# Optimization experiments

Hardware: AMD Instinct MI355X
Metric: run time of the kernel (lower is better)

Reference implementation:

```python
import math
import jax, jax.numpy as jnp
import numpy as np

B, L, DIM, H = 2, 2048, 1024, 16
D = DIM // H  # head_dim = 64
EPS = 1e-6


def setup_inputs() -> dict:
    key = jax.random.key(0)
    ks = jax.random.split(key, 5)
    s = 0.02
    return {
        "x": jax.random.normal(ks[0], (B, L, DIM), jnp.float32),
        "pe": jax.random.normal(ks[1], (B, 1, L, D // 2, 2, 2), jnp.float32),
        "w_qkv": jax.random.normal(ks[2], (DIM, 3 * DIM), jnp.float32) * s,
        "q_scale": jnp.ones((D,), jnp.float32),
        "k_scale": jnp.ones((D,), jnp.float32),
        "w_proj": jax.random.normal(ks[3], (DIM, DIM), jnp.float32) * s,
        "b_proj": jnp.zeros((DIM,), jnp.float32),
    }


def _rmsnorm(t, scale):
    # flax nnx.RMSNorm: x * rsqrt(mean(x^2) + eps) * scale, over last dim
    var = jnp.mean(jnp.square(t), axis=-1, keepdims=True)
    return t * jax.lax.rsqrt(var + EPS) * scale


def _apply_rope(t, pe):
    # t: [B,H,L,D]; pe: [B,1,L,D/2,2,2]
    t2 = t.reshape(*t.shape[:-1], D // 2, 1, 2)
    out = pe[..., 0] * t2[..., 0] + pe[..., 1] * t2[..., 1]  # [B,H,L,D/2,2]
    return out.reshape(t.shape)


def reference(x, pe, w_qkv, q_scale, k_scale, w_proj, b_proj):
    # fused QKV projection
    qkv = jnp.einsum('bld,de->ble', x, w_qkv)  # [B,L,3*DIM]
    qkv = qkv.reshape(B, L, 3, H, D).transpose(2, 0, 3, 1, 4)  # [3,B,H,L,D]
    q, k, v = qkv[0], qkv[1], qkv[2]
    # QK RMSNorm
    q = _rmsnorm(q, q_scale)
    k = _rmsnorm(k, k_scale)
    # RoPE via pe
    q = _apply_rope(q, pe)
    k = _apply_rope(k, pe)
    # scaled dot product attention
    scores = jnp.einsum('bhqd,bhkd->bhqk', q, k) / math.sqrt(D)
    attn = jax.nn.softmax(scores, axis=-1)
    o = jnp.einsum('bhqk,bhkd->bhqd', attn, v)  # [B,H,L,D]
    o = o.transpose(0, 2, 1, 3).reshape(B, L, DIM)  # B H L D -> B L (H D)
    # output projection
    return jnp.einsum('bld,de->ble', o, w_proj) + b_proj
```

## Files before the change

### kernel.cpp

```cpp
#include <hip/hip_runtime.h>
#include <math.h>

#define BB 2
#define LL 2048
#define DIMM 1024
#define HH 16
#define DD 64
#define QKV_N 3072

typedef unsigned short u16;
typedef unsigned int u32;
typedef __attribute__((ext_vector_type(8))) short short8;
typedef __attribute__((ext_vector_type(4))) float f32x4;

__device__ __forceinline__ float bf2f(u16 h) {
    unsigned u = ((unsigned)h) << 16;
    return __uint_as_float(u);
}
__device__ __forceinline__ u16 f2bf(float f) {
    unsigned u = __float_as_uint(f);
    u += 0x7fffu + ((u >> 16) & 1u);
    return (u16)(u >> 16);
}
__device__ __forceinline__ u32 pack_bf2(float lo, float hi) {
    u32 a = __float_as_uint(hi) + 0x8000u;
    u32 b = __float_as_uint(lo) + 0x8000u;
    return __builtin_amdgcn_perm(a, b, 0x07060302u);
}
__device__ __forceinline__ void gload16(const u16* g, u16* l) {
    __builtin_amdgcn_global_load_lds(
        (const __attribute__((address_space(1))) void*)g,
        (__attribute__((address_space(3))) void*)l, 16, 0, 0);
}

__global__ __launch_bounds__(256) void convx(
    const float* __restrict__ X, u16* __restrict__ Af)
{
    const int g = blockIdx.x * 256 + threadIdx.x;
    const int lane = g & 63;
    const int frag = g >> 6;
    const int rt = frag >> 5;
    const int kts = (frag >> 1) & 15;
    const int ks2 = frag & 1;
    const int R = rt * 16 + (lane & 15);
    const int k = kts * 64 + ks2 * 32 + ((lane >> 4) & 3) * 8;
    float4 a = *(const float4*)&X[(size_t)R * DIMM + k];
    float4 b = *(const float4*)&X[(size_t)R * DIMM + k + 4];
    u16 t[8] = {f2bf(a.x), f2bf(a.y), f2bf(a.z), f2bf(a.w),
                f2bf(b.x), f2bf(b.y), f2bf(b.z), f2bf(b.w)};
    *(uint4*)&Af[(size_t)frag * 512 + lane * 8] = *(uint4*)t;
}

__global__ __launch_bounds__(256) void convt(
    const float* __restrict__ W, u16* __restrict__ Wt, int K, int N, int fragmode)
{
    __shared__ u16 s[64][72];
    const int tid = threadIdx.x;
    const int k0 = blockIdx.x * 64, n0 = blockIdx.y * 64;
#pragma unroll
    for (int t = 0; t < 16; ++t) {
        int flat = t * 256 + tid;
        int kk = flat >> 6, nn = flat & 63;
        s[nn][kk] = f2bf(W[(size_t)(k0 + kk) * N + n0 + nn]);
    }
    __syncthreads();
    if (fragmode) {
        const int kts = k0 >> 6;
        const int kdiv = K >> 6;
#pragma unroll
        for (int t2 = 0; t2 < 2; ++t2) {
            int idx = t2 * 256 + tid;
            int fpart = idx >> 6, lane_s = idx & 63;
            int ct = (n0 >> 4) + (fpart >> 1);
            int ks2 = fpart & 1;
            int nn = (fpart >> 1) * 16 + (lane_s & 15);
            int kk = ks2 * 32 + ((lane_s >> 4) & 3) * 8;
            *(uint4*)&Wt[((size_t)(ct * kdiv + kts) * 2 + ks2) * 512 + lane_s * 8]
                = *(const uint4*)&s[nn][kk];
        }
    } else {
#pragma unroll
        for (int t2 = 0; t2 < 2; ++t2) {
            int chunk = t2 * 256 + tid;
            int nn = chunk >> 3, kc = chunk & 7;
            *(uint4*)&Wt[(size_t)(n0 + nn) * K + k0 + kc * 8] = *(uint4*)&s[nn][kc * 8];
        }
    }
}

template<int REGION>
__global__ __launch_bounds__(256) void gemm_qkv_r(
    const u16* __restrict__ Af, const u16* __restrict__ Bf,
    u16* __restrict__ C, u16* __restrict__ kp, u16* __restrict__ vp,
    const float* __restrict__ pe,
    const float* __restrict__ qs, const float* __restrict__ ks)
{
    __shared__ u16 smem[REGION == 0 ? 128 * 136 : 16384];

    const int tid = threadIdx.x;
    const int wave = tid >> 6, lane = tid & 63;
    const int mIdx = lane & 15, quad = lane >> 4;
    const int wr = wave >> 1, wc = wave & 1;
    const int xcd = blockIdx.x & 7, lid = blockIdx.x >> 3;
    const int m0 = (xcd * 4 + (lid >> 3)) * 128;
    const int nblk = lid & 7;
    const int n0 = REGION * 1024 + nblk * 128;
    const int N = QKV_N;

    const u16* abase = Af + ((size_t)((m0 >> 4) + 4 * wr)) * 16384 + lane * 8;
    const u16* bbase = Bf + ((size_t)((n0 >> 4) + 4 * wc)) * 16384 + lane * 8;

    f32x4 acc[4][4];
#pragma unroll
    for (int a = 0; a < 4; ++a)
#pragma unroll
        for (int b = 0; b < 4; ++b) acc[a][b] = (f32x4){0.f, 0.f, 0.f, 0.f};

    short8 aA[4], bA[4], aB[4], bB[4];
#pragma unroll
    for (int i = 0; i < 4; ++i) {
        aA[i] = *(const short8*)&abase[(size_t)i * 16384];
        bA[i] = *(const short8*)&bbase[(size_t)i * 16384];
    }

    for (int t = 0; t < 16; ++t) {
        const size_t o1 = (size_t)t * 1024 + 512;
#pragma unroll
        for (int i = 0; i < 4; ++i) {
            aB[i] = *(const short8*)&abase[(size_t)i * 16384 + o1];
            bB[i] = *(const short8*)&bbase[(size_t)i * 16384 + o1];
        }
        __builtin_amdgcn_sched_barrier(0);
#pragma unroll
        for (int mt = 0; mt < 4; ++mt)
#pragma unroll
            for (int nt = 0; nt < 4; ++nt)
                acc[mt][nt] = __builtin_amdgcn_mfma_f32_16x16x32_bf16(
                    aA[mt], bA[nt], acc[mt][nt], 0, 0, 0);
        __builtin_amdgcn_sched_barrier(0);
        if (t + 1 < 16) {
            const size_t o0 = (size_t)(t + 1) * 1024;
#pragma unroll
            for (int i = 0; i < 4; ++i) {
                aA[i] = *(const short8*)&abase[(size_t)i * 16384 + o0];
                bA[i] = *(const short8*)&bbase[(size_t)i * 16384 + o0];
            }
        }
        __builtin_amdgcn_sched_barrier(0);
#pragma unroll
        for (int mt = 0; mt < 4; ++mt)
#pragma unroll
            for (int nt = 0; nt < 4; ++nt)
                acc[mt][nt] = __builtin_amdgcn_mfma_f32_16x16x32_bf16(
                    aB[mt], bB[nt], acc[mt][nt], 0, 0, 0);
        __builtin_amdgcn_sched_barrier(0);
    }

    if constexpr (REGION == 2) {
#pragma unroll
        for (int mt = 0; mt < 4; ++mt) {
            const int tl0 = 64 * wr + 16 * mt + 4 * quad;
#pragma unroll
            for (int nt = 0; nt < 4; ++nt) {
                const int d = 16 * nt + mIdx;
                const int lblk = ((wc * 2 + (tl0 >> 6)) * 4 + (d >> 4)) * 2
                                 + ((tl0 >> 5) & 1);
                const int ln = (d & 15) + 16 * ((tl0 >> 3) & 3);
                uint2 pr;
                pr.x = pack_bf2(acc[mt][nt][0], acc[mt][nt][1]);
                pr.y = pack_bf2(acc[mt][nt][2], acc[mt][nt][3]);
                *(uint2*)&smem[lblk * 512 + ln * 8 + (tl0 & 7)] = pr;
            }
        }
        __syncthreads();
        {
            const int b = m0 >> 11;
            const int h0 = nblk * 2;
            const int ktb = (m0 & 2047) >> 6;
#pragma unroll
            for (int g2 = 0; g2 < 4; ++g2) {
                const int bh = b * 16 + h0 + (g2 >> 1);
                const int kt = ktb + (g2 & 1);
                u16* dst = vp + ((size_t)(bh * 32 + kt) * 8) * 512;
                const u16* src = &smem[g2 * 8 * 512];
#pragma unroll
                for (int ps = 0; ps < 2; ++ps) {
                    const int off = (ps * 256 + tid) * 8;
                    *(uint4*)&dst[off] = *(const uint4*)&src[off];
                }
            }
        }
    } else {
        const float* scv = (REGION == 0) ? qs : ks;
        const float pre = (REGION == 0) ? 0.18033688011112042f : 1.0f;
        float scl[4];
#pragma unroll
        for (int nt = 0; nt < 4; ++nt) scl[nt] = scv[16 * nt + mIdx];

#pragma unroll
        for (int mt = 0; mt < 4; ++mt) {
#pragma unroll
            for (int r = 0; r < 4; ++r) {
                float s = 0.f;
#pragma unroll
                for (int nt = 0; nt < 4; ++nt) {
                    float a = acc[mt][nt][r];
                    s += a * a;
                }
                s += __shfl_xor(s, 1);
                s += __shfl_xor(s, 2);
                s += __shfl_xor(s, 4);
                s += __shfl_xor(s, 8);
                float rn = rsqrtf(s * (1.f / 64.f) + 1e-6f);
                const int tl = 64 * wr + 16 * mt + 4 * quad + r;
                const int R = m0 + tl;
                size_t peo = (size_t)R * 128;
#pragma unroll
                for (int nt = 0; nt < 4; ++nt) {
                    float v = acc[mt][nt][r] * rn * scl[nt];
                    float pp = __shfl_xor(v, 1);
                    float2 pw = *(const float2*)&pe[peo + 2 * (16 * nt + mIdx)];
                    float e  = (mIdx & 1) ? pp : v;
                    float od = (mIdx & 1) ? v : pp;
                    u16 val = f2bf((pw.x * e + pw.y * od) * pre);
                    if constexpr (REGION == 0) {
                        smem[tl * 136 + 64 * wc + 16 * nt + mIdx] = val;
                    } else {
                        const int d = 16 * nt + mIdx;
                        const int lblk = ((wc * 2 + (tl >> 6)) * 4 + ((tl >> 4) & 3)) * 2
                                         + (d >> 5);
                        smem[lblk * 512 + ((tl & 15) + 16 * ((d >> 3) & 3)) * 8
                             + (d & 7)] = val;
                    }
                }
            }
        }
        __syncthreads();
        if constexpr (REGION == 0) {
            const int row = tid >> 1, half = tid & 1;
            u16* dst = C + (size_t)(m0 + row) * QKV_N + n0 + half * 64;
            const u16* src = &smem[row * 136 + half * 64];
#pragma unroll
            for (int c = 0; c < 8; ++c)
                *(uint4*)&dst[c * 8] = *(const uint4*)&src[c * 8];
        } else {
            const int b = m0 >> 11;
            const int h0 = nblk * 2;
            const int ktb = (m0 & 2047) >> 6;
#pragma unroll
            for (int g2 = 0; g2 < 4; ++g2) {
                const int bh = b * 16 + h0 + (g2 >> 1);
                const int kt = ktb + (g2 & 1);
                u16* dst = kp + ((size_t)(bh * 32 + kt) * 8) * 512;
                const u16* src = &smem[g2 * 8 * 512];
#pragma unroll
                for (int ps = 0; ps < 2; ++ps) {
                    const int off = (ps * 256 + tid) * 8;
                    *(uint4*)&dst[off] = *(const uint4*)&src[off];
                }
            }
        }
    }
}

__global__ __launch_bounds__(256) void gemm_proj(
    const u16* __restrict__ A, const u16* __restrict__ Bt,
    const float* __restrict__ bias, float* __restrict__ C)
{
    __shared__ u16 smem[2 * 12288];

    const int tid = threadIdx.x;
    const int wave = tid >> 6, lane = tid & 63;
    const int mIdx = lane & 15, quad = lane >> 4;
    const int wr = wave >> 1, wc = wave & 1;
    const int xcd = blockIdx.x & 7, lid = blockIdx.x >> 3;
    const int m0 = (xcd * 8 + (lid >> 3)) * 64;
    const int n0 = (lid & 7) * 128;
    const int N = DIMM, K = DIMM;
    const int lr = lane >> 3, lc = lane & 7;

    f32x4 acc[2][4];
#pragma unroll
    for (int a = 0; a < 2; ++a)
#pragma unroll
        for (int b = 0; b < 4; ++b) acc[a][b] = (f32x4){0.f, 0.f, 0.f, 0.f};

    auto stage = [&](int buf, int k0) {
        u16* sA = smem + buf * 12288;
        u16* sB = sA + 4096;
#pragma unroll
        for (int j = 0; j < 2; ++j) {
            int r0 = 16 * wave + 8 * j + lr;
            gload16(&A[(size_t)(m0 + r0) * K + k0 + 8 * (lc ^ lr)],
                    &sA[(16 * wave + 8 * j) * 64]);
        }
#pragma unroll
        for (int j = 0; j < 4; ++j) {
            int r0 = 32 * wave + 8 * j + lr;
            gload16(&Bt[(size_t)(n0 + r0) * K + k0 + 8 * (lc ^ lr)],
                    &sB[(32 * wave + 8 * j) * 64]);
        }
    };

    stage(0, 0);
    __syncthreads();
    int cur = 0;
    for (int t = 0; t < 16; ++t) {
        if (t + 1 < 16) stage(cur ^ 1, (t + 1) * 64);
        const u16* sA = smem + cur * 12288;
        const u16* sB = sA + 4096;
#pragma unroll
        for (int ks2 = 0; ks2 < 2; ++ks2) {
            short8 af[2], bfr[4];
#pragma unroll
            for (int mt = 0; mt < 2; ++mt) {
                int Ra = 32 * wr + 16 * mt + mIdx;
                af[mt] = *(const short8*)&sA[Ra * 64 + 8 * ((ks2 * 4 + quad) ^ (Ra & 7))];
            }
#pragma unroll
            for (int nt = 0; nt < 4; ++nt) {
                int Rb = 64 * wc + 16 * nt + mIdx;
                bfr[nt] = *(const short8*)&sB[Rb * 64 + 8 * ((ks2 * 4 + quad) ^ (Rb & 7))];
            }
#pragma unroll
            for (int mt = 0; mt < 2; ++mt)
#pragma unroll
                for (int nt = 0; nt < 4; ++nt)
                    acc[mt][nt] = __builtin_amdgcn_mfma_f32_16x16x32_bf16(
                        af[mt], bfr[nt], acc[mt][nt], 0, 0, 0);
        }
        __syncthreads();
        cur ^= 1;
    }

#pragma unroll
    for (int mt = 0; mt < 2; ++mt)
#pragma unroll
        for (int r = 0; r < 4; ++r) {
            int row = m0 + 32 * wr + 16 * mt + quad * 4 + r;
#pragma unroll
            for (int nt = 0; nt < 4; ++nt) {
                int col = n0 + 64 * wc + 16 * nt + mIdx;
                C[(size_t)row * N + col] = acc[mt][nt][r] + bias[col];
            }
        }
}

__global__ __launch_bounds__(256, 2) void attn_mfma(
    const u16* __restrict__ qkv, const u16* __restrict__ kp,
    const u16* __restrict__ vp, u16* __restrict__ o)
{
    __shared__ u16 sP[128 * 64];

    const int tid = threadIdx.x;
    const int wave = tid >> 6;
    const int lane = tid & 63;
    const int mIdx = lane & 15;
    const int quad = lane >> 4;
    const int m7 = mIdx & 7;

    const int bid = ((blockIdx.x & 7) << 6) | (blockIdx.x >> 3);
    const int bh = bid >> 4;
    const int qt = bid & 15;
    const int b = bh >> 4, h = bh & 15;
    const int q0 = qt * 128;

    const u16* kbase = kp + (size_t)bh * 32 * 4096 + lane * 8;
    const u16* vbase = vp + (size_t)bh * 32 * 4096 + lane * 8;

    short8 aq[2][2];
#pragma unroll
    for (int g = 0; g < 2; ++g) {
        const u16* qrow = qkv + (size_t)b * LL * QKV_N + h * 64
                          + (size_t)(q0 + 32 * wave + 16 * g + mIdx) * QKV_N;
        aq[g][0] = *(const short8*)&qrow[quad * 8];
        aq[g][1] = *(const short8*)&qrow[32 + quad * 8];
    }

    const short8 bones = {(short)0x3F80, (short)0x3F80, (short)0x3F80, (short)0x3F80,
                          (short)0x3F80, (short)0x3F80, (short)0x3F80, (short)0x3F80};

    f32x4 Oacc[2][4];
    f32x4 lac[2];
#pragma unroll
    for (int g = 0; g < 2; ++g) {
        lac[g] = (f32x4){0.f, 0.f, 0.f, 0.f};
#pragma unroll
        for (int nb = 0; nb < 4; ++nb) Oacc[g][nb] = (f32x4){0.f, 0.f, 0.f, 0.f};
    }

    const int o0 = 8 * (quad ^ m7);
    const int o1 = 8 * ((quad + 4) ^ m7);
    u16* sPr0 = &sP[(32 * wave + mIdx) * 64];
    u16* sPr1 = &sP[(32 * wave + 16 + mIdx) * 64];

    short8 kfA[8], kfB[8], vf[8];

#pragma unroll
    for (int f = 0; f < 8; ++f) kfA[f] = *(const short8*)&kbase[f * 512];

    auto body = [&](short8* KC, short8* KN, int kt) {
        const size_t tb = (size_t)kt * 4096;
#pragma unroll
        for (int f = 0; f < 8; ++f) vf[f] = *(const short8*)&vbase[tb + f * 512];
        if (kt < 31) {
#pragma unroll
            for (int f = 0; f < 8; ++f) KN[f] = *(const short8*)&kbase[tb + 4096 + f * 512];
        }
        __builtin_amdgcn_sched_barrier(0);

#pragma unroll
        for (int nb = 0; nb < 4; ++nb) {
            const int pofs = (16 * nb + 4 * quad) ^ (8 * m7);
#pragma unroll
            for (int g = 0; g < 2; ++g) {
                f32x4 st = (f32x4){0.f, 0.f, 0.f, 0.f};
                st = __builtin_amdgcn_mfma_f32_16x16x32_bf16(KC[nb * 2 + 0], aq[g][0], st, 0, 0, 0);
                st = __builtin_amdgcn_mfma_f32_16x16x32_bf16(KC[nb * 2 + 1], aq[g][1], st, 0, 0, 0);
                float p0 = exp2f(st[0]), p1 = exp2f(st[1]);
                float p2 = exp2f(st[2]), p3 = exp2f(st[3]);
                uint2 wp;
                wp.x = pack_bf2(p0, p1);
                wp.y = pack_bf2(p2, p3);
                *(uint2*)&((g == 0 ? sPr0 : sPr1)[pofs]) = wp;
            }
        }
        short8 pa00 = *(const short8*)&sPr0[o0];
        short8 pa01 = *(const short8*)&sPr0[o1];
        short8 pa10 = *(const short8*)&sPr1[o0];
        short8 pa11 = *(const short8*)&sPr1[o1];

        lac[0] = __builtin_amdgcn_mfma_f32_16x16x32_bf16(pa00, bones, lac[0], 0, 0, 0);
        lac[0] = __builtin_amdgcn_mfma_f32_16x16x32_bf16(pa01, bones, lac[0], 0, 0, 0);
        lac[1] = __builtin_amdgcn_mfma_f32_16x16x32_bf16(pa10, bones, lac[1], 0, 0, 0);
        lac[1] = __builtin_amdgcn_mfma_f32_16x16x32_bf16(pa11, bones, lac[1], 0, 0, 0);

        __builtin_amdgcn_s_setprio(1);
#pragma unroll
        for (int nb = 0; nb < 4; ++nb) {
            Oacc[0][nb] = __builtin_amdgcn_mfma_f32_16x16x32_bf16(pa00, vf[nb * 2 + 0], Oacc[0][nb], 0, 0, 0);
            Oacc[0][nb] = __builtin_amdgcn_mfma_f32_16x16x32_bf16(pa01, vf[nb * 2 + 1], Oacc[0][nb], 0, 0, 0);
            Oacc[1][nb] = __builtin_amdgcn_mfma_f32_16x16x32_bf16(pa10, vf[nb * 2 + 0], Oacc[1][nb], 0, 0, 0);
            Oacc[1][nb] = __builtin_amdgcn_mfma_f32_16x16x32_bf16(pa11, vf[nb * 2 + 1], Oacc[1][nb], 0, 0, 0);
        }
        __builtin_amdgcn_s_setprio(0);
    };

    for (int kt2 = 0; kt2 < 16; ++kt2) {
        body(kfA, kfB, 2 * kt2);
        body(kfB, kfA, 2 * kt2 + 1);
    }

#pragma unroll
    for (int g = 0; g < 2; ++g)
#pragma unroll
        for (int r = 0; r < 4; ++r) {
            float linv = 1.f / lac[g][r];
            const int rowg = b * LL + q0 + 32 * wave + 16 * g + quad * 4 + r;
#pragma unroll
            for (int nb = 0; nb < 4; ++nb) {
                o[(size_t)rowg * DIMM + h * 64 + 16 * nb + mIdx] =
                    f2bf(Oacc[g][nb][r] * linv);
            }
        }
}

extern "C" void kernel_launch(void* const* d_in, const int* in_sizes, int n_in,
                              void* d_out, int out_size, void* d_ws, size_t ws_size,
                              hipStream_t stream) {
    const float* x       = (const float*)d_in[0];
    const float* pe      = (const float*)d_in[1];
    const float* w_qkv   = (const float*)d_in[2];
    const float* q_scale = (const float*)d_in[3];
    const float* k_scale = (const float*)d_in[4];
    const float* w_proj  = (const float*)d_in[5];
    const float* b_proj  = (const float*)d_in[6];
    float* out = (float*)d_out;

    char* ws = (char*)d_ws;
    u16* qkv    = (u16*)ws;  ws += (size_t)4096 * 3072 * 2;
    u16* o      = (u16*)ws;  ws += (size_t)4096 * 1024 * 2;
    u16* xb     = (u16*)ws;  ws += (size_t)4096 * 1024 * 2;
    u16* wqkvt  = (u16*)ws;  ws += (size_t)3072 * 1024 * 2;
    u16* wprojt = (u16*)ws;  ws += (size_t)1024 * 1024 * 2;
    u16* kpack  = (u16*)ws;  ws += (size_t)32 * 32 * 4096 * 2;
    u16* vpack  = (u16*)ws;  ws += (size_t)32 * 32 * 4096 * 2;

    convx<<<(4096 * 1024) / (256 * 8), 256, 0, stream>>>(x, xb);
    convt<<<dim3(1024 / 64, QKV_N / 64), 256, 0, stream>>>(w_qkv, wqkvt, DIMM, QKV_N, 1);
    convt<<<dim3(1024 / 64, 1024 / 64), 256, 0, stream>>>(w_proj, wprojt, DIMM, DIMM, 0);

    gemm_qkv_r<0><<<256, 256, 0, stream>>>(xb, wqkvt, qkv, kpack, vpack, pe, q_scale, k_scale);
    gemm_qkv_r<1><<<256, 256, 0, stream>>>(xb, wqkvt, qkv, kpack, vpack, pe, q_scale, k_scale);
    gemm_qkv_r<2><<<256, 256, 0, stream>>>(xb, wqkvt, qkv, kpack, vpack, pe, q_scale, k_scale);

    attn_mfma<<<BB * HH * (LL / 128), 256, 0, stream>>>(qkv, kpack, vpack, o);

    gemm_proj<<<512, 256, 0, stream>>>(o, wprojt, b_proj, out);
}
```

Measured before the change: 209.5 us.

## Halve attention query tile per block and use hardware bf16 pack conversion

The attention kernel now handles 64 query rows per block (16 per wave) instead of 128. The launch has twice as many blocks, launch bounds request 4 blocks per SM, and register and LDS use per block are halved. The aim is more resident waves to hide the latency of streaming K/V. In exchange, each K/V tile fetched into registers now feeds half as many query rows, which doubles K/V global traffic, and there is less MFMA work to cover each load. Separately, the manual bf16 packing is replaced with the v_cvt_pk_bf16_f32 instruction.

```diff
diff --git a/kernel.cpp b/kernel.cpp
--- a/kernel.cpp
+++ b/kernel.cpp
@@ -26,6 +26,11 @@
     u32 a = __float_as_uint(hi) + 0x8000u;
     u32 b = __float_as_uint(lo) + 0x8000u;
     return __builtin_amdgcn_perm(a, b, 0x07060302u);
+}
+__device__ __forceinline__ u32 cvtpk_bf2(float lo, float hi) {
+    u32 r;
+    asm("v_cvt_pk_bf16_f32 %0, %1, %2" : "=v"(r) : "v"(lo), "v"(hi));
+    return r;
 }
 __device__ __forceinline__ void gload16(const u16* g, u16* l) {
     __builtin_amdgcn_global_load_lds(
@@ -346,11 +351,11 @@
         }
 }
 
-__global__ __launch_bounds__(256, 2) void attn_mfma(
+__global__ __launch_bounds__(256, 4) void attn_mfma(
     const u16* __restrict__ qkv, const u16* __restrict__ kp,
     const u16* __restrict__ vp, u16* __restrict__ o)
 {
-    __shared__ u16 sP[128 * 64];
+    __shared__ u16 sP[64 * 64];
 
     const int tid = threadIdx.x;
     const int wave = tid >> 6;
@@ -359,40 +364,34 @@
     const int quad = lane >> 4;
     const int m7 = mIdx & 7;
 
-    const int bid = ((blockIdx.x & 7) << 6) | (blockIdx.x >> 3);
-    const int bh = bid >> 4;
-    const int qt = bid & 15;
+    const int bid = ((blockIdx.x & 7) << 7) | (blockIdx.x >> 3);
+    const int bh = bid >> 5;
+    const int qt = bid & 31;
     const int b = bh >> 4, h = bh & 15;
-    const int q0 = qt * 128;
+    const int q0 = qt * 64;
 
     const u16* kbase = kp + (size_t)bh * 32 * 4096 + lane * 8;
     const u16* vbase = vp + (size_t)bh * 32 * 4096 + lane * 8;
 
-    short8 aq[2][2];
-#pragma unroll
-    for (int g = 0; g < 2; ++g) {
+    short8 aq0, aq1;
+    {
         const u16* qrow = qkv + (size_t)b * LL * QKV_N + h * 64
-                          + (size_t)(q0 + 32 * wave + 16 * g + mIdx) * QKV_N;
-        aq[g][0] = *(const short8*)&qrow[quad * 8];
-        aq[g][1] = *(const short8*)&qrow[32 + quad * 8];
+                          + (size_t)(q0 + 16 * wave + mIdx) * QKV_N;
+        aq0 = *(const short8*)&qrow[quad * 8];
+        aq1 = *(const short8*)&qrow[32 + quad * 8];
     }
 
     const short8 bones = {(short)0x3F80, (short)0x3F80, (short)0x3F80, (short)0x3F80,
                           (short)0x3F80, (short)0x3F80, (short)0x3F80, (short)0x3F80};
 
-    f32x4 Oacc[2][4];
-    f32x4 lac[2];
-#pragma unroll
-    for (int g = 0; g < 2; ++g) {
-        lac[g] = (f32x4){0.f, 0.f, 0.f, 0.f};
-#pragma unroll
-        for (int nb = 0; nb < 4; ++nb) Oacc[g][nb] = (f32x4){0.f, 0.f, 0.f, 0.f};
-    }
+    f32x4 Oacc[4];
+    f32x4 lac = (f32x4){0.f, 0.f, 0.f, 0.f};
+#pragma unroll
+    for (int nb = 0; nb < 4; ++nb) Oacc[nb] = (f32x4){0.f, 0.f, 0.f, 0.f};
 
     const int o0 = 8 * (quad ^ m7);
     const int o1 = 8 * ((quad + 4) ^ m7);
-    u16* sPr0 = &sP[(32 * wave + mIdx) * 64];
-    u16* sPr1 = &sP[(32 * wave + 16 + mIdx) * 64];
+    u16* sPr = &sP[(16 * wave + mIdx) * 64];
 
     short8 kfA[8], kfB[8], vf[8];
 
@@ -412,36 +411,27 @@
 #pragma unroll
         for (int nb = 0; nb < 4; ++nb) {
             const int pofs = (16 * nb + 4 * quad) ^ (8 * m7);
-#pragma unroll
-            for (int g = 0; g < 2; ++g) {
-                f32x4 st = (f32x4){0.f, 0.f, 0.f, 0.f};
-                st = __builtin_amdgcn_mfma_f32_16x16x32_bf16(KC[nb * 2 + 0], aq[g][0], st, 0, 0, 0);
-                st = __builtin_amdgcn_mfma_f32_16x16x32_bf16(KC[nb * 2 + 1], aq[g][1], st, 0, 0, 0);
-                float p0 = exp2f(st[0]), p1 = exp2f(st[1]);
-                float p2 = exp2f(st[2]), p3 = exp2f(st[3]);
-                uint2 wp;
-                wp.x = pack_bf2(p0, p1);
-                wp.y = pack_bf2(p2, p3);
-                *(uint2*)&((g == 0 ? sPr0 : sPr1)[pofs]) = wp;
-            }
-        }
-        short8 pa00 = *(const short8*)&sPr0[o0];
-        short8 pa01 = *(const short8*)&sPr0[o1];
-        short8 pa10 = *(const short8*)&sPr1[o0];
-        short8 pa11 = *(const short8*)&sPr1[o1];
-
-        lac[0] = __builtin_amdgcn_mfma_f32_16x16x32_bf16(pa00, bones, lac[0], 0, 0, 0);
-        lac[0] = __builtin_amdgcn_mfma_f32_16x16x32_bf16(pa01, bones, lac[0], 0, 0, 0);
-        lac[1] = __builtin_amdgcn_mfma_f32_16x16x32_bf16(pa10, bones, lac[1], 0, 0, 0);
-        lac[1] = __builtin_amdgcn_mfma_f32_16x16x32_bf16(pa11, bones, lac[1], 0, 0, 0);
+            f32x4 st = (f32x4){0.f, 0.f, 0.f, 0.f};
+            st = __builtin_amdgcn_mfma_f32_16x16x32_bf16(KC[nb * 2 + 0], aq0, st, 0, 0, 0);
+            st = __builtin_amdgcn_mfma_f32_16x16x32_bf16(KC[nb * 2 + 1], aq1, st, 0, 0, 0);
+            float p0 = exp2f(st[0]), p1 = exp2f(st[1]);
+            float p2 = exp2f(st[2]), p3 = exp2f(st[3]);
+            uint2 wp;
+            wp.x = cvtpk_bf2(p0, p1);
+            wp.y = cvtpk_bf2(p2, p3);
+            *(uint2*)&sPr[pofs] = wp;
+        }
+        short8 pa0 = *(const short8*)&sPr[o0];
+        short8 pa1 = *(const short8*)&sPr[o1];
+
+        lac = __builtin_amdgcn_mfma_f32_16x16x32_bf16(pa0, bones, lac, 0, 0, 0);
+        lac = __builtin_amdgcn_mfma_f32_16x16x32_bf16(pa1, bones, lac, 0, 0, 0);
 
         __builtin_amdgcn_s_setprio(1);
 #pragma unroll
         for (int nb = 0; nb < 4; ++nb) {
-            Oacc[0][nb] = __builtin_amdgcn_mfma_f32_16x16x32_bf16(pa00, vf[nb * 2 + 0], Oacc[0][nb], 0, 0, 0);
-            Oacc[0][nb] = __builtin_amdgcn_mfma_f32_16x16x32_bf16(pa01, vf[nb * 2 + 1], Oacc[0][nb], 0, 0, 0);
-            Oacc[1][nb] = __builtin_amdgcn_mfma_f32_16x16x32_bf16(pa10, vf[nb * 2 + 0], Oacc[1][nb], 0, 0, 0);
-            Oacc[1][nb] = __builtin_amdgcn_mfma_f32_16x16x32_bf16(pa11, vf[nb * 2 + 1], Oacc[1][nb], 0, 0, 0);
+            Oacc[nb] = __builtin_amdgcn_mfma_f32_16x16x32_bf16(pa0, vf[nb * 2 + 0], Oacc[nb], 0, 0, 0);
+            Oacc[nb] = __builtin_amdgcn_mfma_f32_16x16x32_bf16(pa1, vf[nb * 2 + 1], Oacc[nb], 0, 0, 0);
         }
         __builtin_amdgcn_s_setprio(0);
     };
@@ -452,17 +442,15 @@
     }
 
 #pragma unroll
-    for (int g = 0; g < 2; ++g)
-#pragma unroll
-        for (int r = 0; r < 4; ++r) {
-            float linv = 1.f / lac[g][r];
-            const int rowg = b * LL + q0 + 32 * wave + 16 * g + quad * 4 + r;
-#pragma unroll
-            for (int nb = 0; nb < 4; ++nb) {
-                o[(size_t)rowg * DIMM + h * 64 + 16 * nb + mIdx] =
-                    f2bf(Oacc[g][nb][r] * linv);
-            }
-        }
+    for (int r = 0; r < 4; ++r) {
+        float linv = 1.f / lac[r];
+        const int rowg = b * LL + q0 + 16 * wave + quad * 4 + r;
+#pragma unroll
+        for (int nb = 0; nb < 4; ++nb) {
+            o[(size_t)rowg * DIMM + h * 64 + 16 * nb + mIdx] =
+                f2bf(Oacc[nb][r] * linv);
+        }
+    }
 }
 
 extern "C" void kernel_launch(void* const* d_in, const int* in_sizes, int n_in,
@@ -494,7 +482,7 @@
     gemm_qkv_r<1><<<256, 256, 0, stream>>>(xb, wqkvt, qkv, kpack, vpack, pe, q_scale, k_scale);
     gemm_qkv_r<2><<<256, 256, 0, stream>>>(xb, wqkvt, qkv, kpack, vpack, pe, q_scale, k_scale);
 
-    attn_mfma<<<BB * HH * (LL / 128), 256, 0, stream>>>(qkv, kpack, vpack, o);
+    attn_mfma<<<BB * HH * (LL / 64), 256, 0, stream>>>(qkv, kpack, vpack, o);
 
     gemm_proj<<<512, 256, 0, stream>>>(o, wprojt, b_proj, out);
 }
```

New measurement: 309.1 us. 1.48x slower.
